# Kernel optimization log

Hardware: AMD Instinct MI355X
Metric: run time of the kernel (lower is better)

The kernel has to match this reference:

```python
import jax, jax.numpy as jnp
import numpy as np

B, C, H, W = 4, 3, 1024, 1024
RADII = (8, 16, 32, 64)
EPS = 1e-5  # BatchNorm2d default eps


def _box_sum(x, r, s):
    # depthwise all-ones conv (kernel r, stride s, VALID padding) == summed box
    return jax.lax.reduce_window(x, 0.0, jax.lax.add, (1, 1, r, r), (1, 1, s, s), 'VALID')


def _axis_interp_ac(x, n_out, axis):
    # bilinear (align_corners=True) interpolation along one axis
    n_in = x.shape[axis]
    pos = jnp.arange(n_out, dtype=x.dtype) * ((n_in - 1) / max(n_out - 1, 1))
    i0 = jnp.clip(jnp.floor(pos).astype(jnp.int32), 0, n_in - 2)
    w = pos - i0.astype(x.dtype)
    a = jnp.take(x, i0, axis=axis)
    b = jnp.take(x, i0 + 1, axis=axis)
    shape = [1] * x.ndim
    shape[axis] = n_out
    w = w.reshape(shape)
    return a * (1 - w) + b * w


def _resize_ac(x, oh, ow):
    x = _axis_interp_ac(x, oh, 2)
    x = _axis_interp_ac(x, ow, 3)
    return x


def _bn(x, g, b, rm, rv):
    inv = g / jnp.sqrt(rv + EPS)
    return x * inv[None, :, None, None] + (b - rm * inv)[None, :, None, None]


def _forward(guide, src, w1, g1, b1, rm1, rv1, w2, g2, b2, rm2, rv2, w3):
    Hg, Wg = guide.shape[2], guide.shape[3]
    gg = guide * guide
    gs = guide * src
    ones = jnp.ones((1, guide.shape[1], Hg, Wg), guide.dtype)
    stats = []
    for r in RADII:
        s = r // 2
        N = _box_sum(ones, r, s)
        mx = _box_sum(guide, r, s) / N
        my = _box_sum(src, r, s) / N
        cov = _box_sum(gs, r, s) / N - mx * my
        var = _box_sum(gg, r, s) / N - mx * mx
        stats.append((mx, my, cov, var))
    mx1, my1, cov1, var1 = stats[0]
    oh, ow = cov1.shape[2], cov1.shape[3]
    feats = [cov1, var1]
    for (_, _, cov, var) in stats[1:]:
        feats.append(_resize_ac(cov, oh, ow))
        feats.append(_resize_ac(var, oh, ow))
    x = jnp.concatenate(feats, axis=1)  # [B,24,oh,ow]
    x = jax.nn.relu(_bn(jnp.einsum('oc,bchw->bohw', w1, x), g1, b1, rm1, rv1))
    x = jax.nn.relu(_bn(jnp.einsum('oc,bchw->bohw', w2, x), g2, b2, rm2, rv2))
    A = jnp.einsum('oc,bchw->bohw', w3, x)  # [B,3,oh,ow]
    bb = my1 - A * mx1
    mean_A = _resize_ac(A, Hg, Wg)
    mean_b = _resize_ac(bb, Hg, Wg)
    return mean_A * guide + mean_b


def setup_inputs() -> dict:
    key = jax.random.key(0)
    ks = jax.random.split(key, 5)
    f32 = jnp.float32
    return {
        'guide': jax.random.normal(ks[0], (B, C, H, W), f32),
        'src': jax.random.normal(ks[1], (B, C, H, W), f32),
        'w1': jax.random.normal(ks[2], (48, 24), f32) * 0.05,
        'g1': jnp.ones((48,), f32), 'b1': jnp.zeros((48,), f32),
        'rm1': jnp.zeros((48,), f32), 'rv1': jnp.ones((48,), f32),
        'w2': jax.random.normal(ks[3], (48, 48), f32) * 0.05,
        'g2': jnp.ones((48,), f32), 'b2': jnp.zeros((48,), f32),
        'rm2': jnp.zeros((48,), f32), 'rv2': jnp.ones((48,), f32),
        'w3': jax.random.normal(ks[4], (3, 48), f32) * 0.05,
    }


def reference(guide, src, w1, g1, b1, rm1, rv1, w2, g2, b2, rm2, rv2, w3):
    return _forward(guide, src, w1, g1, b1, rm1, rv1, w2, g2, b2, rm2, rv2, w3)
```

## Files before the change

### kernel.cpp

```cpp
#include <hip/hip_runtime.h>

typedef float v2f __attribute__((ext_vector_type(2)));

#define HH 1024
#define WW 1024
#define NB 4
#define NC 3
#define BC 12
#define N1 255
#define N2 127
#define N3 63
#define N4 31
#define EPS 1e-5f
#define NPIX (NB * N1 * N1)
#define NPAIR (NPIX / 2)

constexpr size_t S8_OFF = 0;
constexpr size_t S8_SZ  = 4ull * BC * N1 * N1;
constexpr size_t CV16_OFF = S8_OFF + S8_SZ;
constexpr size_t CV16_SZ  = 2ull * BC * N2 * N2;
constexpr size_t CV32_OFF = CV16_OFF + CV16_SZ;
constexpr size_t CV32_SZ  = 2ull * BC * N3 * N3;
constexpr size_t CV64_OFF = CV32_OFF + CV32_SZ;
constexpr size_t CV64_SZ  = 2ull * BC * N4 * N4;
constexpr size_t AB_OFF = CV64_OFF + CV64_SZ;

__global__ __launch_bounds__(256) void base_kernel(
    const float* __restrict__ guide, const float* __restrict__ src,
    float4* __restrict__ S8q)
{
    __shared__ float smem[8][WW];

    int b  = blockIdx.x % 128;
    int bc = blockIdx.x / 128;
    int t  = threadIdx.x;

    const float* gbase = guide + (size_t)bc * HH * WW + 4 * t;
    const float* sbase = src   + (size_t)bc * HH * WW + 4 * t;

    float pg[3][4], ps[3][4], pgg[3][4], pgs[3][4];
#pragma unroll
    for (int grp = 0; grp < 3; ++grp)
#pragma unroll
        for (int k = 0; k < 4; ++k) {
            pg[grp][k] = 0.f; ps[grp][k] = 0.f;
            pgg[grp][k] = 0.f; pgs[grp][k] = 0.f;
        }

#pragma unroll
    for (int grp = 0; grp < 3; ++grp) {
#pragma unroll
        for (int r = 0; r < 4; ++r) {
            int row = 8 * b + 4 * grp + r;
            if (row < HH) {
                float4 g4 = *(const float4*)(gbase + (size_t)row * WW);
                float4 s4 = *(const float4*)(sbase + (size_t)row * WW);
                float ge[4] = {g4.x, g4.y, g4.z, g4.w};
                float se[4] = {s4.x, s4.y, s4.z, s4.w};
#pragma unroll
                for (int k = 0; k < 4; ++k) {
                    pg[grp][k]  += ge[k];
                    ps[grp][k]  += se[k];
                    pgg[grp][k] += ge[k] * ge[k];
                    pgs[grp][k] += ge[k] * se[k];
                }
            }
        }
    }

#pragma unroll
    for (int k = 0; k < 4; ++k) {
        int c = 4 * t + k;
        smem[0][c] = pg[0][k]  + pg[1][k];
        smem[1][c] = ps[0][k]  + ps[1][k];
        smem[2][c] = pgg[0][k] + pgg[1][k];
        smem[3][c] = pgs[0][k] + pgs[1][k];
        smem[4][c] = pg[1][k]  + pg[2][k];
        smem[5][c] = ps[1][k]  + ps[2][k];
        smem[6][c] = pgg[1][k] + pgg[2][k];
        smem[7][c] = pgs[1][k] + pgs[2][k];
    }
    __syncthreads();

    if (t < N1) {
        size_t plane = (size_t)bc * N1 * N1;
#pragma unroll
        for (int rsel = 0; rsel < 2; ++rsel) {
            int i = 2 * b + rsel;
            if (i < N1) {
                float qv[4];
#pragma unroll
                for (int q = 0; q < 4; ++q) {
                    const float* arr = smem[4 * rsel + q];
                    float4 a4 = *(const float4*)(arr + 4 * t);
                    float4 b4 = *(const float4*)(arr + 4 * t + 4);
                    qv[q] = (a4.x + a4.y) + (a4.z + a4.w) +
                            (b4.x + b4.y) + (b4.z + b4.w);
                }
                float4 o4; o4.x = qv[0]; o4.y = qv[1]; o4.z = qv[2]; o4.w = qv[3];
                S8q[plane + (size_t)i * N1 + t] = o4;
            }
        }
    }
}

__global__ __launch_bounds__(256) void pyr_all(
    const float4* __restrict__ S8q, v2f* __restrict__ CV16,
    v2f* __restrict__ CV32, v2f* __restrict__ CV64)
{
    const int n2t = BC * N2 * N2, n3t = BC * N3 * N3, n4t = BC * N4 * N4;
    int idx = blockIdx.x * 256 + threadIdx.x;

    v2f* CV; int nout, cnt; float invN; int rem;
    if (idx < n2t)              { CV = CV16; nout = N2; cnt = 2; invN = 1.f / 256.f;  rem = idx; }
    else if (idx < n2t + n3t)   { CV = CV32; nout = N3; cnt = 4; invN = 1.f / 1024.f; rem = idx - n2t; }
    else if (idx < n2t + n3t + n4t) { CV = CV64; nout = N4; cnt = 8; invN = 1.f / 4096.f; rem = idx - n2t - n3t; }
    else return;

    int j  = rem % nout;
    int tt = rem / nout;
    int i  = tt % nout;
    int bc = tt / nout;

    const float4* P = S8q + (size_t)bc * N1 * N1;
    int p0 = cnt * i, q0 = cnt * j;

    float s0 = 0.f, s1 = 0.f, s2 = 0.f, s3 = 0.f;
    for (int ky = 0; ky < cnt; ++ky) {
        size_t roff = (size_t)(p0 + 2 * ky) * N1 + q0;
        for (int kx = 0; kx < cnt; ++kx) {
            float4 q4 = P[roff + 2 * kx];
            s0 += q4.x; s1 += q4.y; s2 += q4.z; s3 += q4.w;
        }
    }

    size_t o = (size_t)bc * nout * nout + (size_t)i * nout + j;
    float mx = s0 * invN, my = s1 * invN;
    v2f cv; cv[0] = s3 * invN - mx * my; cv[1] = s2 * invN - mx * mx;
    CV[o] = cv;
}

__global__ __launch_bounds__(256) void mlp_kernel(
    const float4* __restrict__ S8q,
    const v2f* __restrict__ CV16, const v2f* __restrict__ CV32,
    const v2f* __restrict__ CV64,
    const float* __restrict__ w1, const float* __restrict__ g1,
    const float* __restrict__ b1, const float* __restrict__ rm1,
    const float* __restrict__ rv1,
    const float* __restrict__ w2, const float* __restrict__ g2,
    const float* __restrict__ b2, const float* __restrict__ rm2,
    const float* __restrict__ rv2,
    const float* __restrict__ w3,
    v2f* __restrict__ AB)
{
    __shared__ float4 sw1q[288], sw2q[576], sw3q[36];
    __shared__ float inv1[48], bia1[48], inv2[48], bia2[48];
    int t = threadIdx.x;
    {
        const float4* w1q = (const float4*)w1;
        const float4* w2q = (const float4*)w2;
        const float4* w3q = (const float4*)w3;
        for (int k = t; k < 288; k += 256) sw1q[k] = w1q[k];
        for (int k = t; k < 576; k += 256) sw2q[k] = w2q[k];
        if (t < 36) sw3q[t] = w3q[t];
        if (t < 48) {
            float iv = g1[t] * rsqrtf(rv1[t] + EPS);
            inv1[t] = iv; bia1[t] = b1[t] - rm1[t] * iv;
            float iv2 = g2[t] * rsqrtf(rv2[t] + EPS);
            inv2[t] = iv2; bia2[t] = b2[t] - rm2[t] * iv2;
        }
    }
    __syncthreads();

    int gid = blockIdx.x * 256 + t;
    if (gid >= NPAIR) return;

    float fA[24], fB[24], mxs[2][3], mys[2][3];
    int bs[2], inpl[2];

    const float scales[3] = {(float)(126.0 / 254.0), (float)(62.0 / 254.0),
                             (float)(30.0 / 254.0)};

#pragma unroll
    for (int s = 0; s < 2; ++s) {
        int pidx = 2 * gid + s;
        int ox = pidx % N1;
        int r  = pidx / N1;
        int oy = r % N1;
        int b  = r / N1;
        bs[s] = b; inpl[s] = oy * N1 + ox;
        float* f = s ? fB : fA;

#pragma unroll
        for (int c = 0; c < 3; ++c) {
            float4 q4 = S8q[(size_t)(b * 3 + c) * N1 * N1 + (size_t)oy * N1 + ox];
            float mx = q4.x * (1.f / 64.f), my = q4.y * (1.f / 64.f);
            mxs[s][c] = mx; mys[s][c] = my;
            f[c]     = q4.w * (1.f / 64.f) - mx * my;
            f[3 + c] = q4.z * (1.f / 64.f) - mx * mx;
        }

        const v2f* CVs[3] = {CV16, CV32, CV64};
        const int nins[3] = {N2, N3, N4};
#pragma unroll
        for (int l = 0; l < 3; ++l) {
            const v2f* CV = CVs[l];
            int nin = nins[l];
            float sc = scales[l];
            float py = (float)oy * sc;
            int   i0 = min(max((int)floorf(py), 0), nin - 2);
            float wy = py - (float)i0;
            float px = (float)ox * sc;
            int   j0 = min(max((int)floorf(px), 0), nin - 2);
            float wx = px - (float)j0;
            int fo = 6 + 6 * l;
#pragma unroll
            for (int c = 0; c < 3; ++c) {
                size_t o00 = (size_t)(b * 3 + c) * nin * nin + (size_t)i0 * nin + j0;
                v2f c00 = CV[o00], c01 = CV[o00 + 1];
                v2f c10 = CV[o00 + nin], c11 = CV[o00 + nin + 1];
                v2f res = (c00 * (1.f - wy) + c10 * wy) * (1.f - wx) +
                          (c01 * (1.f - wy) + c11 * wy) * wx;
                f[fo + c]     = res[0];
                f[fo + 3 + c] = res[1];
            }
        }
    }

    v2f f2[24];
#pragma unroll
    for (int c = 0; c < 24; ++c) { f2[c][0] = fA[c]; f2[c][1] = fB[c]; }

    v2f h1[48];
#pragma unroll
    for (int o = 0; o < 48; ++o) {
        const float4* wr = &sw1q[o * 6];
        v2f acc = {0.f, 0.f};
#pragma unroll
        for (int k = 0; k < 6; ++k) {
            float4 wq = wr[k];
            acc += (v2f){wq.x, wq.x} * f2[4 * k + 0];
            acc += (v2f){wq.y, wq.y} * f2[4 * k + 1];
            acc += (v2f){wq.z, wq.z} * f2[4 * k + 2];
            acc += (v2f){wq.w, wq.w} * f2[4 * k + 3];
        }
        float iv = inv1[o], bb = bia1[o];
        v2f h; h[0] = fmaxf(acc[0] * iv + bb, 0.f); h[1] = fmaxf(acc[1] * iv + bb, 0.f);
        h1[o] = h;
    }
    v2f h2[48];
#pragma unroll
    for (int o = 0; o < 48; ++o) {
        const float4* wr = &sw2q[o * 12];
        v2f acc = {0.f, 0.f};
#pragma unroll
        for (int k = 0; k < 12; ++k) {
            float4 wq = wr[k];
            acc += (v2f){wq.x, wq.x} * h1[4 * k + 0];
            acc += (v2f){wq.y, wq.y} * h1[4 * k + 1];
            acc += (v2f){wq.z, wq.z} * h1[4 * k + 2];
            acc += (v2f){wq.w, wq.w} * h1[4 * k + 3];
        }
        float iv = inv2[o], bb = bia2[o];
        v2f h; h[0] = fmaxf(acc[0] * iv + bb, 0.f); h[1] = fmaxf(acc[1] * iv + bb, 0.f);
        h2[o] = h;
    }
#pragma unroll
    for (int c = 0; c < 3; ++c) {
        const float4* wr = &sw3q[c * 12];
        v2f acc = {0.f, 0.f};
#pragma unroll
        for (int k = 0; k < 12; ++k) {
            float4 wq = wr[k];
            acc += (v2f){wq.x, wq.x} * h2[4 * k + 0];
            acc += (v2f){wq.y, wq.y} * h2[4 * k + 1];
            acc += (v2f){wq.z, wq.z} * h2[4 * k + 2];
            acc += (v2f){wq.w, wq.w} * h2[4 * k + 3];
        }
        v2f outA; outA[0] = acc[0]; outA[1] = mys[0][c] - acc[0] * mxs[0][c];
        v2f outB; outB[0] = acc[1]; outB[1] = mys[1][c] - acc[1] * mxs[1][c];
        AB[(size_t)(bs[0] * 3 + c) * N1 * N1 + inpl[0]] = outA;
        AB[(size_t)(bs[1] * 3 + c) * N1 * N1 + inpl[1]] = outB;
    }
}

__global__ __launch_bounds__(256) void final_kernel(
    const float* __restrict__ guide, const v2f* __restrict__ AB,
    float* __restrict__ out)
{
    __shared__ v2f abH[N1 + 1];
    int blk = blockIdx.x;
    int bc  = blk / HH;
    int h   = blk % HH;

    const float scale = (float)(254.0 / 1023.0);
    float py = (float)h * scale;
    int   i0 = min(max((int)floorf(py), 0), N1 - 2);
    float wy = py - (float)i0;

    int t = threadIdx.x;
    if (t < N1) {
        size_t base = (size_t)bc * N1 * N1 + (size_t)i0 * N1 + t;
        v2f p0 = AB[base], p1 = AB[base + N1];
        abH[t] = p0 * (1.f - wy) + p1 * wy;
    }
    __syncthreads();

    const float* gp = guide + (size_t)bc * HH * WW + (size_t)h * WW;
    float*       op = out   + (size_t)bc * HH * WW + (size_t)h * WW;

    float4 g4 = *(const float4*)(gp + 4 * t);
    float ge[4] = {g4.x, g4.y, g4.z, g4.w};
    float oe[4];
#pragma unroll
    for (int k = 0; k < 4; ++k) {
        int w = 4 * t + k;
        float px = (float)w * scale;
        int   j0 = min(max((int)floorf(px), 0), N1 - 2);
        float wx = px - (float)j0;
        v2f ab = abH[j0] * (1.f - wx) + abH[j0 + 1] * wx;
        oe[k] = ab[0] * ge[k] + ab[1];
    }
    float4 o4; o4.x = oe[0]; o4.y = oe[1]; o4.z = oe[2]; o4.w = oe[3];
    *(float4*)(op + 4 * t) = o4;
}

extern "C" void kernel_launch(void* const* d_in, const int* in_sizes, int n_in,
                              void* d_out, int out_size, void* d_ws, size_t ws_size,
                              hipStream_t stream)
{
    const float* guide = (const float*)d_in[0];
    const float* src   = (const float*)d_in[1];
    const float* w1    = (const float*)d_in[2];
    const float* g1    = (const float*)d_in[3];
    const float* b1    = (const float*)d_in[4];
    const float* rm1   = (const float*)d_in[5];
    const float* rv1   = (const float*)d_in[6];
    const float* w2    = (const float*)d_in[7];
    const float* g2    = (const float*)d_in[8];
    const float* b2    = (const float*)d_in[9];
    const float* rm2   = (const float*)d_in[10];
    const float* rv2   = (const float*)d_in[11];
    const float* w3    = (const float*)d_in[12];
    float*       out   = (float*)d_out;

    float* ws    = (float*)d_ws;
    float4* S8q  = (float4*)(ws + S8_OFF);
    v2f*   CV16  = (v2f*)(ws + CV16_OFF);
    v2f*   CV32  = (v2f*)(ws + CV32_OFF);
    v2f*   CV64  = (v2f*)(ws + CV64_OFF);
    v2f*   AB    = (v2f*)(ws + AB_OFF);

    base_kernel<<<BC * 128, 256, 0, stream>>>(guide, src, S8q);

    {
        int total = BC * (N2 * N2 + N3 * N3 + N4 * N4);
        pyr_all<<<(total + 255) / 256, 256, 0, stream>>>(S8q, CV16, CV32, CV64);
    }

    mlp_kernel<<<(NPAIR + 255) / 256, 256, 0, stream>>>(
        S8q, CV16, CV32, CV64, w1, g1, b1, rm1, rv1, w2, g2, b2, rm2, rv2, w3, AB);

    final_kernel<<<BC * HH, 256, 0, stream>>>(guide, AB, out);
}
```

Measured before the change: 238.0 us.

## Reuse row groups across output rows and restructure MLP to one pixel per thread

The base kernel now makes each block handle 16 input rows and four output rows, reusing overlapping 4-row group sums so fewer rows are loaded twice. The MLP kernel changes from two pixels per thread with weights staged in shared memory to one pixel per thread that reads weights straight from global memory (uniform loads) with paired-channel v2f accumulation. The BatchNorm scale and bias are precomputed once in the pyramid kernel and stored in the workspace. This may raise register pressure and scalar-load traffic in the MLP, while cutting redundant global reads in the base pass.

```diff
diff --git a/kernel.cpp b/kernel.cpp
--- a/kernel.cpp
+++ b/kernel.cpp
@@ -13,7 +13,6 @@
 #define N4 31
 #define EPS 1e-5f
 #define NPIX (NB * N1 * N1)
-#define NPAIR (NPIX / 2)
 
 constexpr size_t S8_OFF = 0;
 constexpr size_t S8_SZ  = 4ull * BC * N1 * N1;
@@ -24,6 +23,8 @@
 constexpr size_t CV64_OFF = CV32_OFF + CV32_SZ;
 constexpr size_t CV64_SZ  = 2ull * BC * N4 * N4;
 constexpr size_t AB_OFF = CV64_OFF + CV64_SZ;
+constexpr size_t AB_SZ  = 2ull * NB * NC * N1 * N1;
+constexpr size_t IB_OFF = AB_OFF + AB_SZ;
 
 __global__ __launch_bounds__(256) void base_kernel(
     const float* __restrict__ guide, const float* __restrict__ src,
@@ -31,27 +32,21 @@
 {
     __shared__ float smem[8][WW];
 
-    int b  = blockIdx.x % 128;
-    int bc = blockIdx.x / 128;
+    int b  = blockIdx.x % 64;
+    int bc = blockIdx.x / 64;
     int t  = threadIdx.x;
 
     const float* gbase = guide + (size_t)bc * HH * WW + 4 * t;
     const float* sbase = src   + (size_t)bc * HH * WW + 4 * t;
 
-    float pg[3][4], ps[3][4], pgg[3][4], pgs[3][4];
-#pragma unroll
-    for (int grp = 0; grp < 3; ++grp)
-#pragma unroll
-        for (int k = 0; k < 4; ++k) {
-            pg[grp][k] = 0.f; ps[grp][k] = 0.f;
-            pgg[grp][k] = 0.f; pgs[grp][k] = 0.f;
-        }
-
-#pragma unroll
-    for (int grp = 0; grp < 3; ++grp) {
+    auto load_grp = [&](int g, float c[4][4]) {
+#pragma unroll
+        for (int q = 0; q < 4; ++q)
+#pragma unroll
+            for (int k = 0; k < 4; ++k) c[q][k] = 0.f;
 #pragma unroll
         for (int r = 0; r < 4; ++r) {
-            int row = 8 * b + 4 * grp + r;
+            int row = 16 * b + 4 * g + r;
             if (row < HH) {
                 float4 g4 = *(const float4*)(gbase + (size_t)row * WW);
                 float4 s4 = *(const float4*)(sbase + (size_t)row * WW);
@@ -59,55 +54,81 @@
                 float se[4] = {s4.x, s4.y, s4.z, s4.w};
 #pragma unroll
                 for (int k = 0; k < 4; ++k) {
-                    pg[grp][k]  += ge[k];
-                    ps[grp][k]  += se[k];
-                    pgg[grp][k] += ge[k] * ge[k];
-                    pgs[grp][k] += ge[k] * se[k];
+                    c[0][k] += ge[k];
+                    c[1][k] += se[k];
+                    c[2][k] += ge[k] * ge[k];
+                    c[3][k] += ge[k] * se[k];
                 }
             }
         }
-    }
-
-#pragma unroll
-    for (int k = 0; k < 4; ++k) {
-        int c = 4 * t + k;
-        smem[0][c] = pg[0][k]  + pg[1][k];
-        smem[1][c] = ps[0][k]  + ps[1][k];
-        smem[2][c] = pgg[0][k] + pgg[1][k];
-        smem[3][c] = pgs[0][k] + pgs[1][k];
-        smem[4][c] = pg[1][k]  + pg[2][k];
-        smem[5][c] = ps[1][k]  + ps[2][k];
-        smem[6][c] = pgg[1][k] + pgg[2][k];
-        smem[7][c] = pgs[1][k] + pgs[2][k];
-    }
+    };
+
+    auto store_combo = [&](int rowsel, const float a[4][4], const float bb[4][4]) {
+#pragma unroll
+        for (int q = 0; q < 4; ++q) {
+            float4 v;
+            v.x = a[q][0] + bb[q][0];
+            v.y = a[q][1] + bb[q][1];
+            v.z = a[q][2] + bb[q][2];
+            v.w = a[q][3] + bb[q][3];
+            *(float4*)&smem[rowsel * 4 + q][4 * t] = v;
+        }
+    };
+
+    auto emit = [&](int rowsel, int i) {
+        if (t < N1 && i < N1) {
+            float qv[4];
+#pragma unroll
+            for (int q = 0; q < 4; ++q) {
+                const float* arr = smem[rowsel * 4 + q];
+                float4 a4 = *(const float4*)(arr + 4 * t);
+                float4 b4 = *(const float4*)(arr + 4 * t + 4);
+                qv[q] = (a4.x + a4.y) + (a4.z + a4.w) +
+                        (b4.x + b4.y) + (b4.z + b4.w);
+            }
+            float4 o4; o4.x = qv[0]; o4.y = qv[1]; o4.z = qv[2]; o4.w = qv[3];
+            S8q[(size_t)bc * N1 * N1 + (size_t)i * N1 + t] = o4;
+        }
+    };
+
+    float c0[4][4], c1[4][4], c2[4][4];
+    load_grp(0, c0);
+    load_grp(1, c1);
+    load_grp(2, c2);
+    store_combo(0, c0, c1);
+    store_combo(1, c1, c2);
     __syncthreads();
-
-    if (t < N1) {
-        size_t plane = (size_t)bc * N1 * N1;
-#pragma unroll
-        for (int rsel = 0; rsel < 2; ++rsel) {
-            int i = 2 * b + rsel;
-            if (i < N1) {
-                float qv[4];
-#pragma unroll
-                for (int q = 0; q < 4; ++q) {
-                    const float* arr = smem[4 * rsel + q];
-                    float4 a4 = *(const float4*)(arr + 4 * t);
-                    float4 b4 = *(const float4*)(arr + 4 * t + 4);
-                    qv[q] = (a4.x + a4.y) + (a4.z + a4.w) +
-                            (b4.x + b4.y) + (b4.z + b4.w);
-                }
-                float4 o4; o4.x = qv[0]; o4.y = qv[1]; o4.z = qv[2]; o4.w = qv[3];
-                S8q[plane + (size_t)i * N1 + t] = o4;
-            }
-        }
-    }
+    emit(0, 4 * b + 0);
+    emit(1, 4 * b + 1);
+    __syncthreads();
+    load_grp(3, c1);
+    load_grp(4, c0);
+    store_combo(0, c2, c1);
+    store_combo(1, c1, c0);
+    __syncthreads();
+    emit(0, 4 * b + 2);
+    emit(1, 4 * b + 3);
 }
 
 __global__ __launch_bounds__(256) void pyr_all(
     const float4* __restrict__ S8q, v2f* __restrict__ CV16,
-    v2f* __restrict__ CV32, v2f* __restrict__ CV64)
-{
+    v2f* __restrict__ CV32, v2f* __restrict__ CV64,
+    const float* __restrict__ g1, const float* __restrict__ b1,
+    const float* __restrict__ rm1, const float* __restrict__ rv1,
+    const float* __restrict__ g2, const float* __restrict__ b2,
+    const float* __restrict__ rm2, const float* __restrict__ rv2,
+    float* __restrict__ invbia)
+{
+    if (blockIdx.x == 0 && threadIdx.x < 48) {
+        int o = threadIdx.x;
+        float iv = g1[o] * rsqrtf(rv1[o] + EPS);
+        invbia[o]      = iv;
+        invbia[48 + o] = b1[o] - rm1[o] * iv;
+        float iv2 = g2[o] * rsqrtf(rv2[o] + EPS);
+        invbia[96 + o]  = iv2;
+        invbia[144 + o] = b2[o] - rm2[o] * iv2;
+    }
+
     const int n2t = BC * N2 * N2, n3t = BC * N3 * N3, n4t = BC * N4 * N4;
     int idx = blockIdx.x * 256 + threadIdx.x;
 
@@ -144,143 +165,95 @@
     const float4* __restrict__ S8q,
     const v2f* __restrict__ CV16, const v2f* __restrict__ CV32,
     const v2f* __restrict__ CV64,
-    const float* __restrict__ w1, const float* __restrict__ g1,
-    const float* __restrict__ b1, const float* __restrict__ rm1,
-    const float* __restrict__ rv1,
-    const float* __restrict__ w2, const float* __restrict__ g2,
-    const float* __restrict__ b2, const float* __restrict__ rm2,
-    const float* __restrict__ rv2,
-    const float* __restrict__ w3,
+    const float* __restrict__ w1, const float* __restrict__ w2,
+    const float* __restrict__ w3, const float* __restrict__ invbia,
     v2f* __restrict__ AB)
 {
-    __shared__ float4 sw1q[288], sw2q[576], sw3q[36];
-    __shared__ float inv1[48], bia1[48], inv2[48], bia2[48];
-    int t = threadIdx.x;
-    {
-        const float4* w1q = (const float4*)w1;
-        const float4* w2q = (const float4*)w2;
-        const float4* w3q = (const float4*)w3;
-        for (int k = t; k < 288; k += 256) sw1q[k] = w1q[k];
-        for (int k = t; k < 576; k += 256) sw2q[k] = w2q[k];
-        if (t < 36) sw3q[t] = w3q[t];
-        if (t < 48) {
-            float iv = g1[t] * rsqrtf(rv1[t] + EPS);
-            inv1[t] = iv; bia1[t] = b1[t] - rm1[t] * iv;
-            float iv2 = g2[t] * rsqrtf(rv2[t] + EPS);
-            inv2[t] = iv2; bia2[t] = b2[t] - rm2[t] * iv2;
-        }
-    }
-    __syncthreads();
-
-    int gid = blockIdx.x * 256 + t;
-    if (gid >= NPAIR) return;
-
-    float fA[24], fB[24], mxs[2][3], mys[2][3];
-    int bs[2], inpl[2];
-
+    int idx = blockIdx.x * 256 + threadIdx.x;
+    if (idx >= NPIX) return;
+    int ox = idx % N1;
+    int r  = idx / N1;
+    int oy = r % N1;
+    int b  = r / N1;
+
+    float feats[24], mx1[3], my1[3];
+
+#pragma unroll
+    for (int c = 0; c < 3; ++c) {
+        float4 q4 = S8q[(size_t)(b * 3 + c) * N1 * N1 + (size_t)oy * N1 + ox];
+        float mx = q4.x * (1.f / 64.f), my = q4.y * (1.f / 64.f);
+        mx1[c] = mx; my1[c] = my;
+        feats[c]     = q4.w * (1.f / 64.f) - mx * my;
+        feats[3 + c] = q4.z * (1.f / 64.f) - mx * mx;
+    }
+
+    const v2f* CVs[3]   = {CV16, CV32, CV64};
+    const int nins[3]   = {N2, N3, N4};
     const float scales[3] = {(float)(126.0 / 254.0), (float)(62.0 / 254.0),
                              (float)(30.0 / 254.0)};
-
-#pragma unroll
-    for (int s = 0; s < 2; ++s) {
-        int pidx = 2 * gid + s;
-        int ox = pidx % N1;
-        int r  = pidx / N1;
-        int oy = r % N1;
-        int b  = r / N1;
-        bs[s] = b; inpl[s] = oy * N1 + ox;
-        float* f = s ? fB : fA;
-
+#pragma unroll
+    for (int l = 0; l < 3; ++l) {
+        const v2f* CV = CVs[l];
+        int nin = nins[l];
+        float sc = scales[l];
+        float py = (float)oy * sc;
+        int   i0 = min(max((int)floorf(py), 0), nin - 2);
+        float wy = py - (float)i0;
+        float px = (float)ox * sc;
+        int   j0 = min(max((int)floorf(px), 0), nin - 2);
+        float wx = px - (float)j0;
+        int fo = 6 + 6 * l;
 #pragma unroll
         for (int c = 0; c < 3; ++c) {
-            float4 q4 = S8q[(size_t)(b * 3 + c) * N1 * N1 + (size_t)oy * N1 + ox];
-            float mx = q4.x * (1.f / 64.f), my = q4.y * (1.f / 64.f);
-            mxs[s][c] = mx; mys[s][c] = my;
-            f[c]     = q4.w * (1.f / 64.f) - mx * my;
-            f[3 + c] = q4.z * (1.f / 64.f) - mx * mx;
-        }
-
-        const v2f* CVs[3] = {CV16, CV32, CV64};
-        const int nins[3] = {N2, N3, N4};
-#pragma unroll
-        for (int l = 0; l < 3; ++l) {
-            const v2f* CV = CVs[l];
-            int nin = nins[l];
-            float sc = scales[l];
-            float py = (float)oy * sc;
-            int   i0 = min(max((int)floorf(py), 0), nin - 2);
-            float wy = py - (float)i0;
-            float px = (float)ox * sc;
-            int   j0 = min(max((int)floorf(px), 0), nin - 2);
-            float wx = px - (float)j0;
-            int fo = 6 + 6 * l;
-#pragma unroll
-            for (int c = 0; c < 3; ++c) {
-                size_t o00 = (size_t)(b * 3 + c) * nin * nin + (size_t)i0 * nin + j0;
-                v2f c00 = CV[o00], c01 = CV[o00 + 1];
-                v2f c10 = CV[o00 + nin], c11 = CV[o00 + nin + 1];
-                v2f res = (c00 * (1.f - wy) + c10 * wy) * (1.f - wx) +
-                          (c01 * (1.f - wy) + c11 * wy) * wx;
-                f[fo + c]     = res[0];
-                f[fo + 3 + c] = res[1];
-            }
-        }
-    }
-
-    v2f f2[24];
-#pragma unroll
-    for (int c = 0; c < 24; ++c) { f2[c][0] = fA[c]; f2[c][1] = fB[c]; }
-
-    v2f h1[48];
+            size_t o00 = (size_t)(b * 3 + c) * nin * nin + (size_t)i0 * nin + j0;
+            v2f c00 = CV[o00], c01 = CV[o00 + 1];
+            v2f c10 = CV[o00 + nin], c11 = CV[o00 + nin + 1];
+            v2f res = (c00 * (1.f - wy) + c10 * wy) * (1.f - wx) +
+                      (c01 * (1.f - wy) + c11 * wy) * wx;
+            feats[fo + c]     = res[0];
+            feats[fo + 3 + c] = res[1];
+        }
+    }
+
+    v2f f2[12];
+#pragma unroll
+    for (int k = 0; k < 12; ++k) { f2[k][0] = feats[2 * k]; f2[k][1] = feats[2 * k + 1]; }
+
+    v2f h1v[24];
 #pragma unroll
     for (int o = 0; o < 48; ++o) {
-        const float4* wr = &sw1q[o * 6];
         v2f acc = {0.f, 0.f};
 #pragma unroll
-        for (int k = 0; k < 6; ++k) {
-            float4 wq = wr[k];
-            acc += (v2f){wq.x, wq.x} * f2[4 * k + 0];
-            acc += (v2f){wq.y, wq.y} * f2[4 * k + 1];
-            acc += (v2f){wq.z, wq.z} * f2[4 * k + 2];
-            acc += (v2f){wq.w, wq.w} * f2[4 * k + 3];
-        }
-        float iv = inv1[o], bb = bia1[o];
-        v2f h; h[0] = fmaxf(acc[0] * iv + bb, 0.f); h[1] = fmaxf(acc[1] * iv + bb, 0.f);
-        h1[o] = h;
-    }
-    v2f h2[48];
+        for (int k = 0; k < 12; ++k) {
+            v2f wv = *(const v2f*)(w1 + o * 24 + 2 * k);
+            acc += wv * f2[k];
+        }
+        float v = fmaxf((acc[0] + acc[1]) * invbia[o] + invbia[48 + o], 0.f);
+        h1v[o >> 1][o & 1] = v;
+    }
+    v2f h2v[24];
 #pragma unroll
     for (int o = 0; o < 48; ++o) {
-        const float4* wr = &sw2q[o * 12];
         v2f acc = {0.f, 0.f};
 #pragma unroll
-        for (int k = 0; k < 12; ++k) {
-            float4 wq = wr[k];
-            acc += (v2f){wq.x, wq.x} * h1[4 * k + 0];
-            acc += (v2f){wq.y, wq.y} * h1[4 * k + 1];
-            acc += (v2f){wq.z, wq.z} * h1[4 * k + 2];
-            acc += (v2f){wq.w, wq.w} * h1[4 * k + 3];
-        }
-        float iv = inv2[o], bb = bia2[o];
-        v2f h; h[0] = fmaxf(acc[0] * iv + bb, 0.f); h[1] = fmaxf(acc[1] * iv + bb, 0.f);
-        h2[o] = h;
+        for (int k = 0; k < 24; ++k) {
+            v2f wv = *(const v2f*)(w2 + o * 48 + 2 * k);
+            acc += wv * h1v[k];
+        }
+        float v = fmaxf((acc[0] + acc[1]) * invbia[96 + o] + invbia[144 + o], 0.f);
+        h2v[o >> 1][o & 1] = v;
     }
 #pragma unroll
     for (int c = 0; c < 3; ++c) {
-        const float4* wr = &sw3q[c * 12];
         v2f acc = {0.f, 0.f};
 #pragma unroll
-        for (int k = 0; k < 12; ++k) {
-            float4 wq = wr[k];
-            acc += (v2f){wq.x, wq.x} * h2[4 * k + 0];
-            acc += (v2f){wq.y, wq.y} * h2[4 * k + 1];
-            acc += (v2f){wq.z, wq.z} * h2[4 * k + 2];
-            acc += (v2f){wq.w, wq.w} * h2[4 * k + 3];
-        }
-        v2f outA; outA[0] = acc[0]; outA[1] = mys[0][c] - acc[0] * mxs[0][c];
-        v2f outB; outB[0] = acc[1]; outB[1] = mys[1][c] - acc[1] * mxs[1][c];
-        AB[(size_t)(bs[0] * 3 + c) * N1 * N1 + inpl[0]] = outA;
-        AB[(size_t)(bs[1] * 3 + c) * N1 * N1 + inpl[1]] = outB;
+        for (int k = 0; k < 24; ++k) {
+            v2f wv = *(const v2f*)(w3 + c * 48 + 2 * k);
+            acc += wv * h2v[k];
+        }
+        float a = acc[0] + acc[1];
+        v2f ab; ab[0] = a; ab[1] = my1[c] - a * mx1[c];
+        AB[(size_t)(b * 3 + c) * N1 * N1 + (size_t)oy * N1 + ox] = ab;
     }
 }
 
@@ -350,16 +323,18 @@
     v2f*   CV32  = (v2f*)(ws + CV32_OFF);
     v2f*   CV64  = (v2f*)(ws + CV64_OFF);
     v2f*   AB    = (v2f*)(ws + AB_OFF);
-
-    base_kernel<<<BC * 128, 256, 0, stream>>>(guide, src, S8q);
+    float* invbia = ws + IB_OFF;
+
+    base_kernel<<<BC * 64, 256, 0, stream>>>(guide, src, S8q);
 
     {
         int total = BC * (N2 * N2 + N3 * N3 + N4 * N4);
-        pyr_all<<<(total + 255) / 256, 256, 0, stream>>>(S8q, CV16, CV32, CV64);
-    }
-
-    mlp_kernel<<<(NPAIR + 255) / 256, 256, 0, stream>>>(
-        S8q, CV16, CV32, CV64, w1, g1, b1, rm1, rv1, w2, g2, b2, rm2, rv2, w3, AB);
+        pyr_all<<<(total + 255) / 256, 256, 0, stream>>>(
+            S8q, CV16, CV32, CV64, g1, b1, rm1, rv1, g2, b2, rm2, rv2, invbia);
+    }
+
+    mlp_kernel<<<(NPIX + 255) / 256, 256, 0, stream>>>(
+        S8q, CV16, CV32, CV64, w1, w2, w3, invbia, AB);
 
     final_kernel<<<BC * HH, 256, 0, stream>>>(guide, AB, out);
 }
```

Measured after the change: 245.1 us. 3.0% more time.
